# Kernel tuning notes

Hardware: AMD Instinct MI355X
Metric: run time of the kernel (lower is better)

## Reference

```python
import jax, jax.numpy as jnp
import numpy as np

HEADS, DIM_HEAD, DIM = 8, 64, 512
INNER = HEADS * DIM_HEAD  # 512


def setup_inputs() -> dict:
    key = jax.random.key(0)
    k1, k2, k3 = jax.random.split(key, 3)
    b, n = 2, 2048
    x = jax.random.normal(k1, (b, n, DIM), dtype=jnp.float32)
    # to_qkv: Linear(dim, 4*inner_dim, bias=False); weight stored [out, in]
    w_qkv = jax.random.normal(k2, (4 * INNER, DIM), dtype=jnp.float32) * (1.0 / np.sqrt(DIM))
    # to_out: Linear(2*inner_dim, dim) with bias
    w_out = jax.random.normal(k3, (DIM, 2 * INNER), dtype=jnp.float32) * (1.0 / np.sqrt(2 * INNER))
    b_out = jnp.zeros((DIM,), dtype=jnp.float32)
    return {"x": x, "w_qkv": w_qkv, "w_out": w_out, "b_out": b_out}


def reference(x, w_qkv, w_out, b_out):
    b, n, d = x.shape
    qkvt = x @ w_qkv.T  # [b, n, 4*inner]
    q, k, v, t = jnp.split(qkvt, 4, axis=-1)

    def split_heads(z):
        return z.reshape(b, n, HEADS, DIM_HEAD).transpose(0, 2, 1, 3)  # [b,h,n,dh]

    q, k, v, t = map(split_heads, (q, k, v, t))

    scale = DIM_HEAD ** -0.5
    dots = jnp.einsum('bhid,bhjd->bhij', q, k) * scale
    attn1 = jax.nn.softmax(dots, axis=-1)

    # fixed positional-decay attention: exp(-|i-j|/e), torch broadcast-normalized
    idx = jnp.arange(1, n + 1, dtype=x.dtype)  # linspace(1, n, n)
    tg = jnp.abs(idx[None, :] - idx[:, None])  # [n, n]
    a2 = jnp.exp(-tg / jnp.exp(jnp.asarray(1.0, x.dtype)))
    a2 = a2 / a2.sum(-1)  # broadcasts over last axis, as in the torch code

    out1 = jnp.einsum('bhij,bhjd->bhid', attn1, v)
    out2 = jnp.einsum('ij,bhjd->bhid', a2, t)
    out = jnp.concatenate([out1, out2], axis=-1)  # [b,h,n,2*dh]
    out = out.transpose(0, 2, 1, 3).reshape(b, n, HEADS * 2 * DIM_HEAD)  # [b,n,2*inner]
    return out @ w_out.T + b_out
```

## Files before the change

kernel.cpp:

```cpp
#include <hip/hip_runtime.h>
#include <hip/hip_bf16.h>
#include <stdint.h>

typedef unsigned short u16;
typedef __bf16 bf16;
typedef __bf16 bf16x8 __attribute__((ext_vector_type(8)));
typedef float f32x4 __attribute__((ext_vector_type(4)));
typedef float f32x16 __attribute__((ext_vector_type(16)));

#define NSEQ 2048
#define NDH 64
#define NH 8
#define QKS 2097152ull

__device__ __forceinline__ float b2f(u16 u) {
  union { float f; uint32_t i; } x; x.i = ((uint32_t)u) << 16; return x.f;
}
__device__ __forceinline__ u16 f2b(float f) {
  union { float f; uint32_t i; } x; x.f = f;
  const uint32_t r = x.i + 0x7FFFu + ((x.i >> 16) & 1u);
  return (u16)(r >> 16);
}
__device__ __forceinline__ uint32_t b2pk(float a, float b) {
  union { __hip_bfloat162 h; uint32_t u; } x;
  x.h = __float22bfloat162_rn(make_float2(a, b));
  return x.u;
}
__device__ __forceinline__ void gl16(const void* g, void* l) {
  __builtin_amdgcn_global_load_lds(
      (const __attribute__((address_space(1))) void*)g,
      (__attribute__((address_space(3))) void*)l, 16, 0, 0);
}

__global__ __launch_bounds__(256) void k_cvt(
    const float* __restrict__ X, const float* __restrict__ Wq,
    const float* __restrict__ Wo, u16* __restrict__ Xb,
    u16* __restrict__ Wqb, u16* __restrict__ Wob) {
  const int b = blockIdx.x;
  const float* src; u16* dst; int idx;
  if (b < 1024)      { src = X;  dst = Xb;  idx = b; }
  else if (b < 1536) { src = Wq; dst = Wqb; idx = b - 1024; }
  else               { src = Wo; dst = Wob; idx = b - 1536; }
  const size_t off = ((size_t)idx * 256 + threadIdx.x) * 8;
  const float4 a = *(const float4*)(src + off);
  const float4 c = *(const float4*)(src + off + 4);
  uint4 o = {b2pk(a.x, a.y), b2pk(a.z, a.w), b2pk(c.x, c.y), b2pk(c.z, c.w)};
  *(uint4*)(dst + off) = o;
}

__global__ __launch_bounds__(256) void k_gemm_qkvt(
    const u16* __restrict__ Xb, const u16* __restrict__ Wb, u16* __restrict__ qkvt) {
  __shared__ __align__(16) bf16 smem[18432];
  bf16* A0e = smem;
  bf16* A1e = smem + 4096;
  bf16* B0e = smem + 8192;
  bf16* B1e = smem + 12288;
  const int tid = threadIdx.x;
  const int m0 = blockIdx.x * 128;
  const int n0 = blockIdx.y * 128;
  const int w = tid >> 6, lane = tid & 63;
  const int wy = w >> 1, wx = w & 1;
  const int quad = lane >> 4, l15 = lane & 15;
  const int srow = tid >> 2, sc8 = (tid & 3) * 8;
  const u16* ag = Xb + (size_t)(m0 + srow) * 512 + sc8;
  const u16* bg = Wb + (size_t)(n0 + srow) * 512 + sc8;
  char* aL00 = (char*)smem + w * 1024;
  char* aL01 = (char*)smem + 4096  + w * 1024;
  char* aL10 = (char*)smem + 8192  + w * 1024;
  char* aL11 = (char*)smem + 12288 + w * 1024;
  char* bL00 = (char*)smem + 16384 + w * 1024;
  char* bL01 = (char*)smem + 20480 + w * 1024;
  char* bL10 = (char*)smem + 24576 + w * 1024;
  char* bL11 = (char*)smem + 28672 + w * 1024;
  f32x4 acc[4][4];
#pragma unroll
  for (int mt = 0; mt < 4; ++mt)
#pragma unroll
    for (int nt = 0; nt < 4; ++nt) acc[mt][nt] = (f32x4){0.f, 0.f, 0.f, 0.f};
  for (int kc = 0; kc < 512; kc += 64) {
    __syncthreads();
    gl16(ag + kc,                 aL00);
    gl16(ag + kc + 64 * 512,      aL01);
    gl16(ag + kc + 32,            aL10);
    gl16(ag + kc + 32 + 64 * 512, aL11);
    gl16(bg + kc,                 bL00);
    gl16(bg + kc + 64 * 512,      bL01);
    gl16(bg + kc + 32,            bL10);
    gl16(bg + kc + 32 + 64 * 512, bL11);
    __syncthreads();
#pragma unroll
    for (int ks = 0; ks < 2; ++ks) {
      const bf16* Ae = ks ? A1e : A0e;
      const bf16* Be = ks ? B1e : B0e;
      bf16x8 afr[4], bfr[4];
#pragma unroll
      for (int mt = 0; mt < 4; ++mt)
        afr[mt] = *(const bf16x8*)&Ae[(wy * 64 + mt * 16 + l15) * 32 + quad * 8];
#pragma unroll
      for (int nt = 0; nt < 4; ++nt)
        bfr[nt] = *(const bf16x8*)&Be[(wx * 64 + nt * 16 + l15) * 32 + quad * 8];
#pragma unroll
      for (int mt = 0; mt < 4; ++mt)
#pragma unroll
        for (int nt = 0; nt < 4; ++nt)
          acc[mt][nt] = __builtin_amdgcn_mfma_f32_16x16x32_bf16(afr[mt], bfr[nt], acc[mt][nt], 0, 0, 0);
    }
  }
  __syncthreads();
  const int cbase = n0 + wx * 64;
  const int which = cbase >> 9;
  const int h     = (cbase >> 6) & 7;
  const float scale = (which == 0) ? 0.18033688011112043f : 1.0f;
  bf16* Cw = smem + w * 4608;
  if (which == 2) {
#pragma unroll
    for (int nt = 0; nt < 4; ++nt)
#pragma unroll
      for (int mt = 0; mt < 4; ++mt)
#pragma unroll
        for (int r = 0; r < 4; ++r)
          Cw[(nt * 16 + l15) * 72 + mt * 16 + quad * 4 + r] = (bf16)acc[mt][nt][r];
  } else {
#pragma unroll
    for (int mt = 0; mt < 4; ++mt)
#pragma unroll
      for (int nt = 0; nt < 4; ++nt)
#pragma unroll
        for (int r = 0; r < 4; ++r)
          Cw[(mt * 16 + quad * 4 + r) * 72 + nt * 16 + l15] = (bf16)(acc[mt][nt][r] * scale);
  }
  const int mb = m0 + wy * 64;
  const int bb = mb >> 11;
  const int nn0 = mb & (NSEQ - 1);
  if (which == 2) {
    u16* vt = qkvt + 2ull * QKS + (size_t)(bb * NH + h) * NDH * NSEQ;
#pragma unroll
    for (int p = 0; p < 8; ++p) {
      const int d = p * 8 + (lane >> 3);
      const int t8 = (lane & 7) * 8;
      const uint4 v = *(const uint4*)&Cw[d * 72 + t8];
      *(uint4*)(vt + (size_t)d * NSEQ + nn0 + t8) = v;
    }
  } else {
    u16* dst = qkvt + (size_t)which * QKS + ((size_t)(bb * NH + h) * NSEQ + nn0) * NDH;
#pragma unroll
    for (int p = 0; p < 8; ++p) {
      const int tok = p * 8 + (lane >> 3);
      const int c8 = (lane & 7) * 8;
      const uint4 v = *(const uint4*)&Cw[tok * 72 + c8];
      *(uint4*)(dst + (size_t)tok * NDH + c8) = v;
    }
  }
}

__global__ __launch_bounds__(256) void k_attn_band(
    const u16* __restrict__ qkvt, u16* __restrict__ out12) {
  __shared__ __align__(16) char usmem[72704];
  const int tid = threadIdx.x;
  const int bid = blockIdx.x;
  if (bid >= 128) {
    bf16* Qs = (bf16*)usmem;
    bf16* KV = Qs + 4608;
    bf16* Pw = KV + 9216;
    float* Lpart = (float*)(usmem + 46080);
    bf16* Ks = KV;
    bf16* Vt = KV + 64 * 72;
    const int bh  = bid & 15;
    const int q0  = ((bid - 128) >> 4) * 64;
    const size_t base  = (size_t)bh * (NSEQ * NDH);
    const size_t vbase = 2ull * QKS + (size_t)bh * (NDH * NSEQ);
    const int wq = tid >> 6, lane = tid & 63;
    const int qh = wq >> 1, kh = wq & 1;
    const int l31 = lane & 31, hi = lane >> 5;
    const int srow = tid >> 2, sc0 = (tid & 3) * 16;
    {
      const u16* qp = qkvt + base + (size_t)(q0 + srow) * NDH + sc0;
      *(uint4*)&Qs[srow * 72 + sc0]     = *(const uint4*)qp;
      *(uint4*)&Qs[srow * 72 + sc0 + 8] = *(const uint4*)(qp + 8);
    }
    __syncthreads();
    bf16x8 qb[4];
#pragma unroll
    for (int c = 0; c < 4; ++c)
      qb[c] = *(const bf16x8*)&Qs[(qh * 32 + l31) * 72 + c * 16 + hi * 8];
    float lacc = 0.f;
    f32x16 o[2];
#pragma unroll
    for (int nt = 0; nt < 2; ++nt)
#pragma unroll
      for (int r = 0; r < 16; ++r) o[nt][r] = 0.f;
    const u16* kp = qkvt + QKS + base + (size_t)srow * NDH + sc0;
    const u16* vp = qkvt + vbase + (size_t)srow * NSEQ + sc0;
    uint4 k0 = *(const uint4*)kp;
    uint4 k1 = *(const uint4*)(kp + 8);
    uint4 v0 = *(const uint4*)vp;
    uint4 v1 = *(const uint4*)(vp + 8);
    for (int kt = 0; kt < 32; ++kt) {
      __syncthreads();
      *(uint4*)&Ks[srow * 72 + sc0]     = k0;
      *(uint4*)&Ks[srow * 72 + sc0 + 8] = k1;
      *(uint4*)&Vt[srow * 72 + sc0]     = v0;
      *(uint4*)&Vt[srow * 72 + sc0 + 8] = v1;
      __syncthreads();
      if (kt < 31) {
        const u16* kn = kp + (size_t)(kt + 1) * 64 * NDH;
        const u16* vn = vp + (kt + 1) * 64;
        k0 = *(const uint4*)kn;
        k1 = *(const uint4*)(kn + 8);
        v0 = *(const uint4*)vn;
        v1 = *(const uint4*)(vn + 8);
      }
      f32x16 s;
#pragma unroll
      for (int r = 0; r < 16; ++r) s[r] = 0.f;
      __builtin_amdgcn_s_setprio(1);
#pragma unroll
      for (int c = 0; c < 4; ++c) {
        const bf16x8 ka = *(const bf16x8*)&Ks[(kh * 32 + l31) * 72 + c * 16 + hi * 8];
        s = __builtin_amdgcn_mfma_f32_32x32x16_bf16(ka, qb[c], s, 0, 0, 0);
      }
      __builtin_amdgcn_s_setprio(0);
      float ts = 0.f;
#pragma unroll
      for (int r = 0; r < 16; ++r) {
        s[r] = __builtin_amdgcn_exp2f(s[r]);
        ts += s[r];
      }
      ts += __shfl_xor(ts, 32);
      lacc += ts;
      bf16* pr = Pw + (wq * 32 + l31) * 72;
#pragma unroll
      for (int g = 0; g < 4; ++g) {
        uint2 t = {b2pk(s[4 * g], s[4 * g + 1]), b2pk(s[4 * g + 2], s[4 * g + 3])};
        *(uint2*)&pr[g * 8 + hi * 4] = t;
      }
      __builtin_amdgcn_s_setprio(1);
#pragma unroll
      for (int c = 0; c < 2; ++c) {
        const bf16x8 pa = *(const bf16x8*)&Pw[(wq * 32 + l31) * 72 + c * 16 + hi * 8];
        const bf16x8 vb0 = *(const bf16x8*)&Vt[l31 * 72 + kh * 32 + c * 16 + hi * 8];
        const bf16x8 vb1 = *(const bf16x8*)&Vt[(32 + l31) * 72 + kh * 32 + c * 16 + hi * 8];
        o[0] = __builtin_amdgcn_mfma_f32_32x32x16_bf16(pa, vb0, o[0], 0, 0, 0);
        o[1] = __builtin_amdgcn_mfma_f32_32x32x16_bf16(pa, vb1, o[1], 0, 0, 0);
      }
      __builtin_amdgcn_s_setprio(0);
    }
    __syncthreads();
    if (lane < 32) Lpart[wq * 32 + lane] = lacc;
    float* Osum = (float*)KV;
    if (kh == 1) {
#pragma unroll
      for (int nt = 0; nt < 2; ++nt)
#pragma unroll
        for (int r = 0; r < 16; ++r) {
          const int row = (r & 3) + 8 * (r >> 2) + 4 * hi;
          Osum[(qh * 32 + row) * 64 + nt * 32 + l31] = o[nt][r];
        }
    }
    __syncthreads();
    if (kh == 0) {
      const int bb = bh >> 3, h = bh & 7;
#pragma unroll
      for (int r = 0; r < 16; ++r) {
        const int row = (r & 3) + 8 * (r >> 2) + 4 * hi;
        const float lt = Lpart[qh * 2 * 32 + row] + Lpart[(qh * 2 + 1) * 32 + row];
        const float inv = 1.f / lt;
        const int nn = q0 + qh * 32 + row;
        u16* dst = out12 + (size_t)(bb * NSEQ + nn) * 1024 + h * 128;
        dst[l31]      = f2b((o[0][r] + Osum[(qh * 32 + row) * 64 + l31]) * inv);
        dst[32 + l31] = f2b((o[1][r] + Osum[(qh * 32 + row) * 64 + 32 + l31]) * inv);
      }
    }
  } else {
    float* sinv = (float*)usmem;
    float* fb   = (float*)(usmem + 3072);
    const int cb = bid;
    const int w = tid >> 6, d = tid & 63;
    const int c  = (cb & 7) * 4 + w;
    const int i0 = c * 64;
    const int bh = cb >> 3;
    const size_t tb = 3ull * QKS + (size_t)bh * (NSEQ * NDH);
    const float EI = 0.36787944117144233f;
    const float RR = 0.69220062755534635f;
    const float OMR = 1.f - RR;
#pragma unroll
    for (int p = 0; p < 3; ++p) {
      const int j = i0 - 64 + p * 64 + d;
      const float r1 = __expf(-(float)(j + 1) * EI);
      const float r2 = __expf(-(float)(NSEQ - j) * EI);
      sinv[w * 192 + p * 64 + d] = OMR / (1.f - r1 + RR - r2);
    }
    const u16* tp = qkvt + tb + d;
    float f = 0.f;
    if (c > 0) {
#pragma unroll 8
      for (int jj = 0; jj < 64; ++jj)
        f = RR * f + sinv[w * 192 + jj] * b2f(tp[(size_t)(i0 - 64 + jj) * NDH]);
    }
#pragma unroll 8
    for (int jj = 0; jj < 64; ++jj) {
      f = RR * f + sinv[w * 192 + 64 + jj] * b2f(tp[(size_t)(i0 + jj) * NDH]);
      fb[(w * 64 + jj) * 68 + d] = f;
    }
    float b = 0.f;
    if (c < 31) {
#pragma unroll 8
      for (int jj = 63; jj >= 0; --jj)
        b = RR * b + sinv[w * 192 + 128 + jj] * b2f(tp[(size_t)(i0 + 64 + jj) * NDH]);
    }
    const int bb = bh >> 3, h = bh & 7;
#pragma unroll 8
    for (int jj = 63; jj >= 0; --jj) {
      const float g = sinv[w * 192 + 64 + jj] * b2f(tp[(size_t)(i0 + jj) * NDH]);
      b = RR * b + g;
      out12[(size_t)(bb * NSEQ + i0 + jj) * 1024 + h * 128 + 64 + d] =
          f2b(fb[(w * 64 + jj) * 68 + d] + b - g);
    }
  }
}

__global__ __launch_bounds__(256) void k_gemm_out(
    const u16* __restrict__ A, const u16* __restrict__ Wb,
    const float* __restrict__ bias, float* __restrict__ out) {
  __shared__ __align__(16) float smemf[6144];
  bf16* A0e = (bf16*)smemf;
  bf16* A1e = (bf16*)smemf + 4096;
  bf16* B0e = (bf16*)smemf + 8192;
  bf16* B1e = (bf16*)smemf + 10240;
  const int tid = threadIdx.x;
  const int m0 = blockIdx.x * 128;
  const int n0 = blockIdx.y * 64;
  const int w = tid >> 6, lane = tid & 63;
  const int wy = w >> 1, wx = w & 1;
  const int quad = lane >> 4, l15 = lane & 15;
  const int srow = tid >> 2, sc8 = (tid & 3) * 8;
  const u16* ap = A  + (size_t)(m0 + srow) * 1024 + sc8;
  const u16* bp = Wb + (size_t)(n0 + srow) * 1024 + sc8;
  char* aL00 = (char*)smemf + w * 1024;
  char* aL01 = (char*)smemf + 4096  + w * 1024;
  char* aL10 = (char*)smemf + 8192  + w * 1024;
  char* aL11 = (char*)smemf + 12288 + w * 1024;
  char* bL0  = (char*)smemf + 16384 + w * 1024;
  char* bL1  = (char*)smemf + 20480 + w * 1024;
  f32x4 acc[4][2];
#pragma unroll
  for (int mt = 0; mt < 4; ++mt)
#pragma unroll
    for (int nt = 0; nt < 2; ++nt) acc[mt][nt] = (f32x4){0.f, 0.f, 0.f, 0.f};
  for (int kc = 0; kc < 1024; kc += 64) {
    __syncthreads();
    gl16(ap + kc,                  aL00);
    gl16(ap + kc + 64 * 1024,      aL01);
    gl16(ap + kc + 32,             aL10);
    gl16(ap + kc + 32 + 64 * 1024, aL11);
    gl16(bp + kc,                  bL0);
    gl16(bp + kc + 32,             bL1);
    __syncthreads();
#pragma unroll
    for (int ks = 0; ks < 2; ++ks) {
      const bf16* Ae = ks ? A1e : A0e;
      const bf16* Be = ks ? B1e : B0e;
      bf16x8 afr[4], bfr[2];
#pragma unroll
      for (int mt = 0; mt < 4; ++mt)
        afr[mt] = *(const bf16x8*)&Ae[(wy * 64 + mt * 16 + l15) * 32 + quad * 8];
#pragma unroll
      for (int nt = 0; nt < 2; ++nt)
        bfr[nt] = *(const bf16x8*)&Be[(wx * 32 + nt * 16 + l15) * 32 + quad * 8];
#pragma unroll
      for (int mt = 0; mt < 4; ++mt)
#pragma unroll
        for (int nt = 0; nt < 2; ++nt)
          acc[mt][nt] = __builtin_amdgcn_mfma_f32_16x16x32_bf16(afr[mt], bfr[nt], acc[mt][nt], 0, 0, 0);
    }
  }
  float bias_v[2];
#pragma unroll
  for (int nt = 0; nt < 2; ++nt) bias_v[nt] = bias[n0 + wx * 32 + nt * 16 + l15];
  __syncthreads();
  float* Cw = smemf + w * 576;
  const int erow = lane >> 2, ec8 = (lane & 3) * 8;
#pragma unroll
  for (int mt = 0; mt < 4; ++mt) {
#pragma unroll
    for (int nt = 0; nt < 2; ++nt)
#pragma unroll
      for (int r = 0; r < 4; ++r)
        Cw[(quad * 4 + r) * 36 + nt * 16 + l15] = acc[mt][nt][r] + bias_v[nt];
    const float4 v0 = *(const float4*)&Cw[erow * 36 + ec8];
    const float4 v1 = *(const float4*)&Cw[erow * 36 + ec8 + 4];
    float* op = out + (size_t)(m0 + wy * 64 + mt * 16 + erow) * 512 + n0 + wx * 32 + ec8;
    *(float4*)op       = v0;
    *(float4*)(op + 4) = v1;
  }
}

extern "C" void kernel_launch(void* const* d_in, const int* in_sizes, int n_in,
                              void* d_out, int out_size, void* d_ws, size_t ws_size,
                              hipStream_t stream) {
  (void)in_sizes; (void)n_in; (void)out_size; (void)ws_size;
  const float* x     = (const float*)d_in[0];
  const float* w_qkv = (const float*)d_in[1];
  const float* w_out = (const float*)d_in[2];
  const float* b_out = (const float*)d_in[3];
  float* out = (float*)d_out;
  u16* ws    = (u16*)d_ws;
  u16* qkvt  = ws;
  u16* out12 = ws + 8ull  * 1024 * 1024;
  u16* Xb    = ws + 12ull * 1024 * 1024;
  u16* Wqb   = ws + 14ull * 1024 * 1024;
  u16* Wob   = ws + 15ull * 1024 * 1024;
  k_cvt      <<<dim3(1792), 256, 0, stream>>>(x, w_qkv, w_out, Xb, Wqb, Wob);
  k_gemm_qkvt<<<dim3(32, 16), 256, 0, stream>>>(Xb, Wqb, qkvt);
  k_attn_band<<<dim3(640), 256, 0, stream>>>(qkvt, out12);
  k_gemm_out <<<dim3(32, 8), 256, 0, stream>>>(out12, Wob, b_out, out);
}
```

Baseline: 143.3 us.

## Keep softmax probabilities and decay scan in registers, shrink attention LDS

The P matrix of the band-attention path is no longer written to and read back from LDS. The MFMA output layout is instead turned into the A-operand layout with lane shuffles across the two half-waves. The decay-filter blocks now keep the forward scan in a fully unrolled 64-entry register array instead of an LDS buffer. LDS use per block drops from about 71 KB to 28 KB, which lets more blocks share a CU, but the register array and full unrolling raise VGPR pressure and could cause spills or lower occupancy.

```diff
diff --git a/kernel.cpp b/kernel.cpp
--- a/kernel.cpp
+++ b/kernel.cpp
@@ -155,14 +155,13 @@
 
 __global__ __launch_bounds__(256) void k_attn_band(
     const u16* __restrict__ qkvt, u16* __restrict__ out12) {
-  __shared__ __align__(16) char usmem[72704];
+  __shared__ __align__(16) char usmem[28160];
   const int tid = threadIdx.x;
   const int bid = blockIdx.x;
   if (bid >= 128) {
     bf16* Qs = (bf16*)usmem;
     bf16* KV = Qs + 4608;
-    bf16* Pw = KV + 9216;
-    float* Lpart = (float*)(usmem + 46080);
+    float* Lpart = (float*)(usmem + 27648);
     bf16* Ks = KV;
     bf16* Vt = KV + 64 * 72;
     const int bh  = bid & 15;
@@ -228,20 +227,28 @@
       }
       ts += __shfl_xor(ts, 32);
       lacc += ts;
-      bf16* pr = Pw + (wq * 32 + l31) * 72;
-#pragma unroll
-      for (int g = 0; g < 4; ++g) {
-        uint2 t = {b2pk(s[4 * g], s[4 * g + 1]), b2pk(s[4 * g + 2], s[4 * g + 3])};
-        *(uint2*)&pr[g * 8 + hi * 4] = t;
-      }
+      const uint32_t w0 = b2pk(s[0], s[1]),   w1 = b2pk(s[2], s[3]);
+      const uint32_t w2 = b2pk(s[4], s[5]),   w3 = b2pk(s[6], s[7]);
+      const uint32_t w4 = b2pk(s[8], s[9]),   w5 = b2pk(s[10], s[11]);
+      const uint32_t w6 = b2pk(s[12], s[13]), w7 = b2pk(s[14], s[15]);
+      const uint32_t e0 = __shfl_xor(hi ? w0 : w2, 32);
+      const uint32_t e1 = __shfl_xor(hi ? w1 : w3, 32);
+      const uint32_t e2 = __shfl_xor(hi ? w4 : w6, 32);
+      const uint32_t e3 = __shfl_xor(hi ? w5 : w7, 32);
+      uint4 u0 = hi ? (uint4){e0, e1, w2, w3} : (uint4){w0, w1, e0, e1};
+      uint4 u1 = hi ? (uint4){e2, e3, w6, w7} : (uint4){w4, w5, e2, e3};
+      const bf16x8 pa0 = *(const bf16x8*)&u0;
+      const bf16x8 pa1 = *(const bf16x8*)&u1;
       __builtin_amdgcn_s_setprio(1);
-#pragma unroll
-      for (int c = 0; c < 2; ++c) {
-        const bf16x8 pa = *(const bf16x8*)&Pw[(wq * 32 + l31) * 72 + c * 16 + hi * 8];
-        const bf16x8 vb0 = *(const bf16x8*)&Vt[l31 * 72 + kh * 32 + c * 16 + hi * 8];
-        const bf16x8 vb1 = *(const bf16x8*)&Vt[(32 + l31) * 72 + kh * 32 + c * 16 + hi * 8];
-        o[0] = __builtin_amdgcn_mfma_f32_32x32x16_bf16(pa, vb0, o[0], 0, 0, 0);
-        o[1] = __builtin_amdgcn_mfma_f32_32x32x16_bf16(pa, vb1, o[1], 0, 0, 0);
+      {
+        const bf16x8 vb00 = *(const bf16x8*)&Vt[l31 * 72        + kh * 32 + hi * 8];
+        const bf16x8 vb10 = *(const bf16x8*)&Vt[(32 + l31) * 72 + kh * 32 + hi * 8];
+        o[0] = __builtin_amdgcn_mfma_f32_32x32x16_bf16(pa0, vb00, o[0], 0, 0, 0);
+        o[1] = __builtin_amdgcn_mfma_f32_32x32x16_bf16(pa0, vb10, o[1], 0, 0, 0);
+        const bf16x8 vb01 = *(const bf16x8*)&Vt[l31 * 72        + kh * 32 + 16 + hi * 8];
+        const bf16x8 vb11 = *(const bf16x8*)&Vt[(32 + l31) * 72 + kh * 32 + 16 + hi * 8];
+        o[0] = __builtin_amdgcn_mfma_f32_32x32x16_bf16(pa1, vb01, o[0], 0, 0, 0);
+        o[1] = __builtin_amdgcn_mfma_f32_32x32x16_bf16(pa1, vb11, o[1], 0, 0, 0);
       }
       __builtin_amdgcn_s_setprio(0);
     }
@@ -273,7 +280,6 @@
     }
   } else {
     float* sinv = (float*)usmem;
-    float* fb   = (float*)(usmem + 3072);
     const int cb = bid;
     const int w = tid >> 6, d = tid & 63;
     const int c  = (cb & 7) * 4 + w;
@@ -291,30 +297,31 @@
       sinv[w * 192 + p * 64 + d] = OMR / (1.f - r1 + RR - r2);
     }
     const u16* tp = qkvt + tb + d;
+    float fr[64];
     float f = 0.f;
     if (c > 0) {
-#pragma unroll 8
+#pragma unroll
       for (int jj = 0; jj < 64; ++jj)
         f = RR * f + sinv[w * 192 + jj] * b2f(tp[(size_t)(i0 - 64 + jj) * NDH]);
     }
-#pragma unroll 8
+#pragma unroll
     for (int jj = 0; jj < 64; ++jj) {
       f = RR * f + sinv[w * 192 + 64 + jj] * b2f(tp[(size_t)(i0 + jj) * NDH]);
-      fb[(w * 64 + jj) * 68 + d] = f;
+      fr[jj] = f;
     }
     float b = 0.f;
     if (c < 31) {
-#pragma unroll 8
+#pragma unroll
       for (int jj = 63; jj >= 0; --jj)
         b = RR * b + sinv[w * 192 + 128 + jj] * b2f(tp[(size_t)(i0 + 64 + jj) * NDH]);
     }
     const int bb = bh >> 3, h = bh & 7;
-#pragma unroll 8
+#pragma unroll
     for (int jj = 63; jj >= 0; --jj) {
       const float g = sinv[w * 192 + 64 + jj] * b2f(tp[(size_t)(i0 + jj) * NDH]);
       b = RR * b + g;
       out12[(size_t)(bb * NSEQ + i0 + jj) * 1024 + h * 128 + 64 + d] =
-          f2b(fb[(w * 64 + jj) * 68 + d] + b - g);
+          f2b(fr[jj] + b - g);
     }
   }
 }
```

Measured after the change: 174.8 us. 1.22x slower.
